# Optimization experiments

Measured on AMD Instinct MI355X. Metric: run time of the kernel, lower is better.

## Reference

```python
import jax, jax.numpy as jnp
import numpy as np

TEMP = 0.07
BASE_TEMP = 0.07
LOSS_WEIGHT = 0.5
BN_EPS = 1e-5


def _embed(x, w1, b1, gamma, beta, w2, b2):
    # 1x1 conv C->C  (x: [N,C,H,W], w1: [C_out,C_in])
    h = jnp.einsum('nchw,oc->nohw', x, w1) + b1[None, :, None, None]
    # BatchNorm2d in training mode: batch stats over (N,H,W), biased variance
    mean = h.mean(axis=(0, 2, 3), keepdims=True)
    var = h.var(axis=(0, 2, 3), keepdims=True)
    h = (h - mean) * jax.lax.rsqrt(var + BN_EPS)
    h = h * gamma[None, :, None, None] + beta[None, :, None, None]
    h = jax.nn.relu(h)
    h = jnp.einsum('nchw,oc->nohw', h, w2) + b2[None, :, None, None]
    # F.normalize(p=2, dim=1) with eps=1e-12
    nrm = jnp.sqrt(jnp.sum(h * h, axis=1, keepdims=True))
    return h / jnp.maximum(nrm, 1e-12)


def _contrastive(feats_, labels_):
    # feats_: [T, n_view, C]; labels_: [T]
    T, n_view, C = feats_.shape
    mask_small = (labels_[:, None] == labels_[None, :]).astype(feats_.dtype)  # [T,T]
    # torch.cat(torch.unbind(feats_, dim=1), dim=0): view-major ordering
    cf = feats_.transpose(1, 0, 2).reshape(T * n_view, C)
    logits = (cf @ cf.T) / TEMP                                   # [M,M], M=T*n_view
    logits = logits - jax.lax.stop_gradient(jnp.max(logits, axis=1, keepdims=True))
    mask = jnp.tile(mask_small, (n_view, n_view))                  # repeat(anchor_count, contrast_count)
    neg_mask = 1.0 - mask                                          # computed BEFORE diagonal removal
    M = T * n_view
    logits_mask = 1.0 - jnp.eye(M, dtype=feats_.dtype)
    mask = mask * logits_mask
    exp_logits = jnp.exp(logits)
    neg_logits = jnp.sum(exp_logits * neg_mask, axis=1, keepdims=True)
    log_prob = logits - jnp.log(exp_logits + neg_logits)
    mean_log_prob_pos = jnp.sum(mask * log_prob, axis=1) / (jnp.sum(mask, axis=1) + 1e-6)
    loss = -(TEMP / BASE_TEMP) * mean_log_prob_pos
    return jnp.mean(loss)


def setup_inputs() -> dict:
    N, C_in, H, W = 8, 512, 128, 128
    feat_dim, num_classes = 256, 19
    max_views, max_samples, ignore_label = 100, 1024, -1
    rng = np.random.RandomState(0)

    preds_S = rng.randn(N, C_in, H, W).astype(np.float32)
    # gt label map already at (H,W) => nearest interpolation is identity
    gt = rng.randint(0, num_classes, (N, H * W))
    logits_S = rng.randn(N, num_classes, H * W).astype(np.float32)
    predict = logits_S.argmax(axis=1)  # [N, H*W]

    # ---- replicate _hard_anchor_sampling on host (fixed seed) ----
    classes, total = [], 0
    for i in range(N):
        cl = [int(c) for c in np.unique(gt[i])
              if c != ignore_label and (gt[i] == c).sum() > max_views]
        classes.append(cl)
        total += len(cl)
    n_view = min(max_samples // total, max_views)

    b_idx, p_idx, y_cls = [], [], []
    for i in range(N):
        for c in classes[i]:
            hard = np.where((predict[i] == c) & (gt[i] != c))[0]
            easy = np.where((predict[i] == c) & (gt[i] == c))[0]
            nh, ne = len(hard), len(easy)
            if nh >= n_view / 2 and ne >= n_view / 2:
                kh = n_view // 2; ke = n_view - kh
            elif nh >= n_view / 2:
                ke = ne; kh = n_view - ke
            else:
                kh = nh; ke = n_view - kh
            hs = hard[rng.permutation(nh)[:kh]]
            es = easy[rng.permutation(ne)[:ke]]
            b_idx.append(i)
            p_idx.append(np.concatenate([hs, es]))
            y_cls.append(c)

    batch_idx = jnp.asarray(np.array(b_idx), dtype=jnp.int32)          # [T]
    pix_idx = jnp.asarray(np.stack(p_idx), dtype=jnp.int32)            # [T, n_view]
    y_cls = jnp.asarray(np.array(y_cls), dtype=jnp.int32)              # [T]

    def p(shape, scale, k):
        r = np.random.RandomState(k)
        return jnp.asarray((r.randn(*shape) * scale).astype(np.float32))

    return {
        'preds_S': jnp.asarray(preds_S),
        'w1': p((C_in, C_in), 0.02, 1),
        'b1': jnp.zeros((C_in,), jnp.float32),
        'gamma': jnp.ones((C_in,), jnp.float32),
        'beta': jnp.zeros((C_in,), jnp.float32),
        'w2': p((feat_dim, C_in), 0.02, 2),
        'b2': jnp.zeros((feat_dim,), jnp.float32),
        'batch_idx': batch_idx,
        'pix_idx': pix_idx,
        'y_cls': y_cls,
    }


def reference(preds_S, w1, b1, gamma, beta, w2, b2, batch_idx, pix_idx, y_cls):
    f = _embed(preds_S, w1, b1, gamma, beta, w2, b2)        # [N, C, H, W]
    N, C, H, W = f.shape
    feats = f.transpose(0, 2, 3, 1).reshape(N, H * W, C)     # [N, HW, C]
    X_ = feats[batch_idx[:, None], pix_idx]                   # [T, n_view, C]
    labels_ = y_cls.astype(f.dtype)
    return LOSS_WEIGHT * _contrastive(X_, labels_)
```

## Files before the change

kernel.cpp:

```cpp
#include <hip/hip_runtime.h>
#include <hip/hip_bf16.h>

#define C_IN   512
#define C_OUT  256
#define HW     16384
#define NIMG   8
#define PTOT   (NIMG * HW)
#define MP     1024
#define TEMP_INV (1.0f / 0.07f)
#define BN_EPS   1e-5f
#define SPB    4
#define OGRP   8
#define IGRP   4

typedef float  f32x4  __attribute__((ext_vector_type(4)));
typedef short  short8 __attribute__((ext_vector_type(8)));
typedef short  short4v __attribute__((ext_vector_type(4)));

#define WS_S1   0
#define WS_G    (WS_S1 + C_IN)
#define WS_W1P  (WS_G + C_IN * C_IN)
#define WS_B1P  (WS_W1P + C_IN * C_IN)
#define WS_CF   (WS_B1P + C_IN)
#define WS_XB_F (WS_CF + MP * C_OUT)
#define WS_NEED_FAST ((size_t)WS_XB_F * 4 + (size_t)PTOT * C_IN * 2)

__global__ __launch_bounds__(256)
void kprep(const float* __restrict__ x, __hip_bfloat16* __restrict__ xb,
           float* __restrict__ s1) {
    int plane = blockIdx.x;
    int c = plane & (C_IN - 1);
    const float4* p = (const float4*)(x + (size_t)plane * HW);
    short4v* q = (short4v*)(xb + (size_t)plane * HW);
    float acc = 0.f;
    for (int i = threadIdx.x; i < HW / 4; i += 256) {
        float4 v = p[i];
        acc += v.x + v.y + v.z + v.w;
        union { short4v s; __hip_bfloat162 h[2]; } u;
        u.h[0] = __float22bfloat162_rn(make_float2(v.x, v.y));
        u.h[1] = __float22bfloat162_rn(make_float2(v.z, v.w));
        q[i] = u.s;
    }
    for (int off = 32; off; off >>= 1) acc += __shfl_down(acc, off, 64);
    __shared__ float red[4];
    int lane = threadIdx.x & 63, wv = threadIdx.x >> 6;
    if (lane == 0) red[wv] = acc;
    __syncthreads();
    if (threadIdx.x == 0)
        atomicAdd(&s1[c], red[0] + red[1] + red[2] + red[3]);
}

__global__ __launch_bounds__(256)
void ksum(const float* __restrict__ x, float* __restrict__ s1) {
    int plane = blockIdx.x;
    int c = plane & (C_IN - 1);
    const float4* p = (const float4*)(x + (size_t)plane * HW);
    float acc = 0.f;
    for (int i = threadIdx.x; i < HW / 4; i += 256) {
        float4 v = p[i];
        acc += v.x + v.y + v.z + v.w;
    }
    for (int off = 32; off; off >>= 1) acc += __shfl_down(acc, off, 64);
    __shared__ float red[4];
    int lane = threadIdx.x & 63, wv = threadIdx.x >> 6;
    if (lane == 0) red[wv] = acc;
    __syncthreads();
    if (threadIdx.x == 0)
        atomicAdd(&s1[c], red[0] + red[1] + red[2] + red[3]);
}

__device__ const int TILE_I[10] = {0,0,0,0,1,1,1,2,2,3};
__device__ const int TILE_J[10] = {0,1,2,3,1,2,3,2,3,3};

__global__ __launch_bounds__(256, 2)
void kgram_bf16(const __hip_bfloat16* __restrict__ xb, float* __restrict__ G) {
    int tile  = blockIdx.x;
    int chunk = blockIdx.y;
    int n   = chunk >> 4;
    int hw0 = (chunk & 15) * 1024;
    int wave = threadIdx.x >> 6;
    int lane = threadIdx.x & 63;
    int wi = wave >> 1, wj = wave & 1;
    int I0 = TILE_I[tile] * 128 + wi * 64;
    int J0 = TILE_J[tile] * 128 + wj * 64;
    int m    = lane & 15;
    int koff = (lane >> 4) * 8;

    const __hip_bfloat16* rowA[4];
    const __hip_bfloat16* rowB[4];
#pragma unroll
    for (int t = 0; t < 4; ++t) {
        rowA[t] = xb + ((size_t)n * C_IN + (I0 + t * 16 + m)) * HW + hw0 + koff;
        rowB[t] = xb + ((size_t)n * C_IN + (J0 + t * 16 + m)) * HW + hw0 + koff;
    }

    f32x4 acc[4][4];
#pragma unroll
    for (int i = 0; i < 4; ++i)
#pragma unroll
        for (int j = 0; j < 4; ++j) acc[i][j] = {0.f, 0.f, 0.f, 0.f};

    short8 A0[4][2], B0[4][2], A1[4][2], B1[4][2];

#define LOADSTAGE(Ab, Bb, kk)                                              \
    {                                                                      \
        _Pragma("unroll")                                                  \
        for (int t = 0; t < 4; ++t) {                                      \
            Ab[t][0] = *(const short8*)(rowA[t] + (kk));                   \
            Ab[t][1] = *(const short8*)(rowA[t] + (kk) + 32);              \
            Bb[t][0] = *(const short8*)(rowB[t] + (kk));                   \
            Bb[t][1] = *(const short8*)(rowB[t] + (kk) + 32);              \
        }                                                                  \
    }
#define MFMASTAGE(Ab, Bb)                                                  \
    {                                                                      \
        _Pragma("unroll")                                                  \
        for (int u = 0; u < 2; ++u)                                        \
            _Pragma("unroll")                                              \
            for (int i = 0; i < 4; ++i)                                    \
                _Pragma("unroll")                                          \
                for (int j = 0; j < 4; ++j)                                \
                    acc[i][j] = __builtin_amdgcn_mfma_f32_16x16x32_bf16(   \
                        Ab[i][u], Bb[j][u], acc[i][j], 0, 0, 0);           \
    }

    LOADSTAGE(A0, B0, 0)
    int kk = 0;
#pragma unroll 1
    for (int s = 0; s < 7; ++s) {
        LOADSTAGE(A1, B1, kk + 64)
        MFMASTAGE(A0, B0)
        LOADSTAGE(A0, B0, kk + 128)
        MFMASTAGE(A1, B1)
        kk += 128;
    }
    LOADSTAGE(A1, B1, kk + 64)
    MFMASTAGE(A0, B0)
    MFMASTAGE(A1, B1)
#undef LOADSTAGE
#undef MFMASTAGE

    int r0 = (lane >> 4) * 4;
    int cc = lane & 15;
#pragma unroll
    for (int i = 0; i < 4; ++i)
#pragma unroll
        for (int j = 0; j < 4; ++j)
#pragma unroll
            for (int r = 0; r < 4; ++r)
                atomicAdd(&G[(size_t)(I0 + i * 16 + r0 + r) * C_IN + (J0 + j * 16 + cc)],
                          acc[i][j][r]);
}

__global__ __launch_bounds__(256)
void kmirror(float* __restrict__ G) {
    int i = blockIdx.x;
    for (int j = threadIdx.x; j < C_IN; j += 256) {
        if ((i >> 7) > (j >> 7))
            G[(size_t)i * C_IN + j] = G[(size_t)j * C_IN + i];
    }
}

__device__ inline short8 load_frag_f32(const float* p) {
    float4 a = *(const float4*)p;
    float4 b = *(const float4*)(p + 4);
    union { short8 s; __hip_bfloat162 h[4]; } u;
    u.h[0] = __float22bfloat162_rn(make_float2(a.x, a.y));
    u.h[1] = __float22bfloat162_rn(make_float2(a.z, a.w));
    u.h[2] = __float22bfloat162_rn(make_float2(b.x, b.y));
    u.h[3] = __float22bfloat162_rn(make_float2(b.z, b.w));
    return u.s;
}

__global__ __launch_bounds__(256)
void kgram_f32(const float* __restrict__ x, float* __restrict__ G) {
    int bz  = blockIdx.z;
    int n   = bz >> 2;
    int hw0 = (bz & 3) * 4096;
    int wave = threadIdx.x >> 6;
    int lane = threadIdx.x & 63;
    int wi = wave >> 1, wj = wave & 1;
    int I0 = blockIdx.x * 128 + wi * 64;
    int J0 = blockIdx.y * 128 + wj * 64;
    int m    = lane & 15;
    int koff = (lane >> 4) * 8;

    const float* baseA[4];
    const float* baseB[4];
#pragma unroll
    for (int t = 0; t < 4; ++t) {
        baseA[t] = x + ((size_t)n * C_IN + (I0 + t * 16 + m)) * HW + hw0 + koff;
        baseB[t] = x + ((size_t)n * C_IN + (J0 + t * 16 + m)) * HW + hw0 + koff;
    }

    f32x4 acc[4][4];
#pragma unroll
    for (int i = 0; i < 4; ++i)
#pragma unroll
        for (int j = 0; j < 4; ++j) acc[i][j] = {0.f, 0.f, 0.f, 0.f};

    for (int kk = 0; kk < 4096; kk += 32) {
        short8 afr[4], bfr[4];
#pragma unroll
        for (int t = 0; t < 4; ++t) {
            afr[t] = load_frag_f32(baseA[t] + kk);
            bfr[t] = load_frag_f32(baseB[t] + kk);
        }
#pragma unroll
        for (int i = 0; i < 4; ++i)
#pragma unroll
            for (int j = 0; j < 4; ++j)
                acc[i][j] = __builtin_amdgcn_mfma_f32_16x16x32_bf16(
                    afr[i], bfr[j], acc[i][j], 0, 0, 0);
    }

    int r0 = (lane >> 4) * 4;
    int cc = lane & 15;
#pragma unroll
    for (int i = 0; i < 4; ++i)
#pragma unroll
        for (int j = 0; j < 4; ++j)
#pragma unroll
            for (int r = 0; r < 4; ++r)
                atomicAdd(&G[(size_t)(I0 + i * 16 + r0 + r) * C_IN + (J0 + j * 16 + cc)],
                          acc[i][j][r]);
}

__global__ __launch_bounds__(256)
void kstats(const float* __restrict__ w1, const float* __restrict__ b1,
            const float* __restrict__ gamma, const float* __restrict__ beta,
            const float* __restrict__ s1, const float* __restrict__ G,
            float* __restrict__ w1p, float* __restrict__ b1p) {
    int o0 = blockIdx.x * OGRP;
    int tid = threadIdx.x;
    __shared__ float wr[OGRP][C_IN];
    __shared__ float redd[4][OGRP];
    __shared__ float redq[4][OGRP];
    __shared__ float alpha_s[OGRP];

    for (int idx = tid; idx < OGRP * C_IN; idx += 256) {
        int og = idx >> 9, c = idx & (C_IN - 1);
        wr[og][c] = w1[(size_t)(o0 + og) * C_IN + c];
    }
    __syncthreads();

    float dot1[OGRP], quad[OGRP];
#pragma unroll
    for (int og = 0; og < OGRP; ++og) { dot1[og] = 0.f; quad[og] = 0.f; }

    for (int c = tid; c < C_IN; c += 256) {
        const float* gr = G + (size_t)c * C_IN;
        float s1c = s1[c];
        float inner[OGRP];
#pragma unroll
        for (int og = 0; og < OGRP; ++og) inner[og] = 0.f;
        for (int d = 0; d < C_IN; d += 4) {
            float4 gv = *(const float4*)(gr + d);
#pragma unroll
            for (int og = 0; og < OGRP; ++og) {
                float4 wv = *(const float4*)(&wr[og][d]);
                inner[og] += gv.x * wv.x + gv.y * wv.y + gv.z * wv.z + gv.w * wv.w;
            }
        }
#pragma unroll
        for (int og = 0; og < OGRP; ++og) {
            float wc = wr[og][c];
            quad[og] += inner[og] * wc;
            dot1[og] += s1c * wc;
        }
    }
#pragma unroll
    for (int og = 0; og < OGRP; ++og) {
        for (int off = 32; off; off >>= 1) {
            dot1[og] += __shfl_down(dot1[og], off, 64);
            quad[og] += __shfl_down(quad[og], off, 64);
        }
    }
    int lane = tid & 63, wv = tid >> 6;
    if (lane == 0) {
#pragma unroll
        for (int og = 0; og < OGRP; ++og) { redd[wv][og] = dot1[og]; redq[wv][og] = quad[og]; }
    }
    __syncthreads();
    if (tid < OGRP) {
        int og = tid;
        float d1 = redd[0][og] + redd[1][og] + redd[2][og] + redd[3][og];
        float q  = redq[0][og] + redq[1][og] + redq[2][og] + redq[3][og];
        float b  = b1[o0 + og];
        float mean = d1 / (float)PTOT + b;
        float eh2  = (q + 2.f * b * d1) / (float)PTOT + b * b;
        float var  = eh2 - mean * mean;
        float al   = gamma[o0 + og] * rsqrtf(var + BN_EPS);
        alpha_s[og] = al;
        b1p[o0 + og] = beta[o0 + og] + al * (b - mean);
    }
    __syncthreads();
    for (int idx = tid; idx < OGRP * C_IN; idx += 256) {
        int og = idx >> 9, c = idx & (C_IN - 1);
        w1p[(size_t)(o0 + og) * C_IN + c] = alpha_s[og] * wr[og][c];
    }
}

__global__ __launch_bounds__(256)
void kfeat(const float* __restrict__ x, const float* __restrict__ w1p,
           const float* __restrict__ b1p, const float* __restrict__ w2,
           const float* __restrict__ b2, const int* __restrict__ batch_idx,
           const int* __restrict__ pix_idx, float* __restrict__ cf,
           int M, int T, int n_view) {
    __shared__ float xcol[SPB][C_IN];
    __shared__ float h1[SPB][C_IN];
    __shared__ float fl[SPB][C_OUT];
    int tid = threadIdx.x;
    int m0 = blockIdx.x * SPB;

    for (int idx = tid; idx < SPB * C_IN; idx += 256) {
        int s = idx >> 9, c = idx & (C_IN - 1);
        int mm = m0 + s;
        float v = 0.f;
        if (mm < M) {
            int t = mm % T, vv = mm / T;
            int n = batch_idx[t];
            int pix = pix_idx[t * n_view + vv];
            v = x[((size_t)n * C_IN + c) * HW + pix];
        }
        xcol[s][c] = v;
    }
    __syncthreads();

    for (int o = tid; o < C_IN; o += 256) {
        float acc[SPB];
        float bb = b1p[o];
#pragma unroll
        for (int s = 0; s < SPB; ++s) acc[s] = bb;
        const float* wrp = w1p + (size_t)o * C_IN;
        for (int c = 0; c < C_IN; ++c) {
            float w = wrp[c];
#pragma unroll
            for (int s = 0; s < SPB; ++s) acc[s] += w * xcol[s][c];
        }
#pragma unroll
        for (int s = 0; s < SPB; ++s) h1[s][o] = fmaxf(acc[s], 0.f);
    }
    __syncthreads();

    {
        int j = tid;
        float acc[SPB];
        float bb = b2[j];
#pragma unroll
        for (int s = 0; s < SPB; ++s) acc[s] = bb;
        const float* wrp = w2 + (size_t)j * C_IN;
        for (int o = 0; o < C_IN; ++o) {
            float w = wrp[o];
#pragma unroll
            for (int s = 0; s < SPB; ++s) acc[s] += w * h1[s][o];
        }
#pragma unroll
        for (int s = 0; s < SPB; ++s) fl[s][j] = acc[s];
    }
    __syncthreads();

    int wv = tid >> 6, lane = tid & 63;
    {
        float sq = 0.f;
#pragma unroll
        for (int k = 0; k < 4; ++k) { float v = fl[wv][lane + 64 * k]; sq += v * v; }
        for (int off = 32; off; off >>= 1) sq += __shfl_down(sq, off, 64);
        float nrm = __shfl(sq, 0, 64);
        float rinv = 1.f / fmaxf(sqrtf(nrm), 1e-12f);
        int mm = m0 + wv;
        if (mm < M) {
#pragma unroll
            for (int k = 0; k < 4; ++k)
                cf[(size_t)mm * C_OUT + lane + 64 * k] = fl[wv][lane + 64 * k] * rinv;
        }
    }
}

__global__ __launch_bounds__(256)
void kloss(const float* __restrict__ cf, const int* __restrict__ y_cls,
           float* __restrict__ out, int M, int T) {
    int i0 = blockIdx.x * IGRP;
    int tid = threadIdx.x;
    __shared__ float ci[IGRP][C_OUT];
    __shared__ float row[IGRP][MP];
    __shared__ int   lbl[MP];
    __shared__ float redl[IGRP];
    int lane = tid & 63, wv = tid >> 6;

    for (int idx = tid; idx < IGRP * C_OUT; idx += 256) {
        int g = idx >> 8, c = idx & (C_OUT - 1);
        int ii = i0 + g;
        ci[g][c] = (ii < M) ? cf[(size_t)ii * C_OUT + c] : 0.f;
    }
    for (int j = tid; j < M; j += 256) lbl[j] = y_cls[j % T];
    __syncthreads();

    for (int j = tid; j < M; j += 256) {
        const float* cj = cf + (size_t)j * C_OUT;
        float acc[IGRP];
#pragma unroll
        for (int g = 0; g < IGRP; ++g) acc[g] = 0.f;
        for (int c = 0; c < C_OUT; c += 4) {
            float4 v = *(const float4*)(cj + c);
#pragma unroll
            for (int g = 0; g < IGRP; ++g) {
                float4 cv = *(const float4*)(&ci[g][c]);
                acc[g] += cv.x * v.x + cv.y * v.y + cv.z * v.z + cv.w * v.w;
            }
        }
#pragma unroll
        for (int g = 0; g < IGRP; ++g) row[g][j] = acc[g] * TEMP_INV;
    }
    __syncthreads();

    int i = i0 + wv;
    if (i < M) {
        int lbl_i = lbl[i];
        const float* r = row[wv];

        float mx = -1e30f;
        for (int j = lane; j < M; j += 64) mx = fmaxf(mx, r[j]);
        for (int off = 32; off; off >>= 1) mx = fmaxf(mx, __shfl_down(mx, off, 64));
        mx = __shfl(mx, 0, 64);

        float neg = 0.f;
        for (int j = lane; j < M; j += 64)
            if (lbl[j] != lbl_i) neg += expf(r[j] - mx);
        for (int off = 32; off; off >>= 1) neg += __shfl_down(neg, off, 64);
        neg = __shfl(neg, 0, 64);

        float pos = 0.f; int cnt = 0;
        for (int j = lane; j < M; j += 64) {
            if (lbl[j] == lbl_i && j != i) {
                float l = r[j] - mx;
                pos += l - logf(expf(l) + neg);
                cnt++;
            }
        }
        for (int off = 32; off; off >>= 1) {
            pos += __shfl_down(pos, off, 64);
            cnt += __shfl_down(cnt, off, 64);
        }
        if (lane == 0) redl[wv] = -pos / ((float)cnt + 1e-6f);
    } else if (lane == 0) redl[wv] = 0.f;
    __syncthreads();
    if (tid == 0) {
        float s = redl[0] + redl[1] + redl[2] + redl[3];
        atomicAdd(out, s * (0.5f / (float)M));
    }
}

extern "C" void kernel_launch(void* const* d_in, const int* in_sizes, int n_in,
                              void* d_out, int out_size, void* d_ws, size_t ws_size,
                              hipStream_t stream) {
    const float* x     = (const float*)d_in[0];
    const float* w1    = (const float*)d_in[1];
    const float* b1    = (const float*)d_in[2];
    const float* gamma = (const float*)d_in[3];
    const float* beta  = (const float*)d_in[4];
    const float* w2    = (const float*)d_in[5];
    const float* b2    = (const float*)d_in[6];
    const int* batch_idx = (const int*)d_in[7];
    const int* pix_idx   = (const int*)d_in[8];
    const int* y_cls     = (const int*)d_in[9];

    int T = in_sizes[7];
    int M = in_sizes[8];
    int n_view = M / T;

    float* ws  = (float*)d_ws;
    float* s1  = ws + WS_S1;
    float* G   = ws + WS_G;
    float* w1p = ws + WS_W1P;
    float* b1p = ws + WS_B1P;
    float* cf  = ws + WS_CF;
    __hip_bfloat16* xb = (__hip_bfloat16*)(ws + WS_XB_F);

    hipMemsetAsync(s1, 0, (size_t)(C_IN + C_IN * C_IN) * sizeof(float), stream);
    hipMemsetAsync(d_out, 0, sizeof(float), stream);

    if (ws_size >= WS_NEED_FAST) {
        kprep<<<NIMG * C_IN, 256, 0, stream>>>(x, xb, s1);
        kgram_bf16<<<dim3(10, 128), 256, 0, stream>>>(xb, G);
        kmirror<<<C_IN, 256, 0, stream>>>(G);
    } else {
        ksum<<<NIMG * C_IN, 256, 0, stream>>>(x, s1);
        kgram_f32<<<dim3(4, 4, 32), 256, 0, stream>>>(x, G);
    }
    kstats<<<C_IN / OGRP, 256, 0, stream>>>(w1, b1, gamma, beta, s1, G, w1p, b1p);
    kfeat<<<(M + SPB - 1) / SPB, 256, 0, stream>>>(x, w1p, b1p, w2, b2,
                                                   batch_idx, pix_idx, cf, M, T, n_view);
    kloss<<<(M + IGRP - 1) / IGRP, 256, 0, stream>>>(cf, y_cls, (float*)d_out, M, T);
}
```

Baseline: 769.9 us.

## Stage Gram tiles through swizzled LDS via direct global-to-LDS loads

The bf16 Gram kernel used to load MFMA fragments straight from global memory into registers, so each wave re-read rows that other waves in the block also needed. It now copies each 128-row A/B tile into double-buffered, XOR-swizzled shared memory with global_load_lds, and the waves read their fragments from LDS. This cuts redundant global traffic but adds a barrier per K step and 64KB of LDS, which may limit occupancy. Separately, the contrastive-loss kernel now handles 8 anchor rows per block instead of 4.

```diff
diff --git a/kernel.cpp b/kernel.cpp
--- a/kernel.cpp
+++ b/kernel.cpp
@@ -11,7 +11,8 @@
 #define BN_EPS   1e-5f
 #define SPB    4
 #define OGRP   8
-#define IGRP   4
+#define IGRP   8
+#define BK     64
 
 typedef float  f32x4  __attribute__((ext_vector_type(4)));
 typedef short  short8 __attribute__((ext_vector_type(8)));
@@ -74,6 +75,8 @@
 
 __global__ __launch_bounds__(256, 2)
 void kgram_bf16(const __hip_bfloat16* __restrict__ xb, float* __restrict__ G) {
+    __shared__ __hip_bfloat16 Abuf[2][128 * BK];
+    __shared__ __hip_bfloat16 Bbuf[2][128 * BK];
     int tile  = blockIdx.x;
     int chunk = blockIdx.y;
     int n   = chunk >> 4;
@@ -81,18 +84,14 @@
     int wave = threadIdx.x >> 6;
     int lane = threadIdx.x & 63;
     int wi = wave >> 1, wj = wave & 1;
-    int I0 = TILE_I[tile] * 128 + wi * 64;
-    int J0 = TILE_J[tile] * 128 + wj * 64;
-    int m    = lane & 15;
-    int koff = (lane >> 4) * 8;
-
-    const __hip_bfloat16* rowA[4];
-    const __hip_bfloat16* rowB[4];
-#pragma unroll
-    for (int t = 0; t < 4; ++t) {
-        rowA[t] = xb + ((size_t)n * C_IN + (I0 + t * 16 + m)) * HW + hw0 + koff;
-        rowB[t] = xb + ((size_t)n * C_IN + (J0 + t * 16 + m)) * HW + hw0 + koff;
-    }
+    int IT = TILE_I[tile] * 128;
+    int JT = TILE_J[tile] * 128;
+
+    const __hip_bfloat16* gA = xb + ((size_t)n * C_IN + IT) * HW + hw0;
+    const __hip_bfloat16* gB = xb + ((size_t)n * C_IN + JT) * HW + hw0;
+
+    int rrel = lane >> 3;
+    int slot = lane & 7;
 
     f32x4 acc[4][4];
 #pragma unroll
@@ -100,45 +99,66 @@
 #pragma unroll
         for (int j = 0; j < 4; ++j) acc[i][j] = {0.f, 0.f, 0.f, 0.f};
 
-    short8 A0[4][2], B0[4][2], A1[4][2], B1[4][2];
-
-#define LOADSTAGE(Ab, Bb, kk)                                              \
-    {                                                                      \
-        _Pragma("unroll")                                                  \
-        for (int t = 0; t < 4; ++t) {                                      \
-            Ab[t][0] = *(const short8*)(rowA[t] + (kk));                   \
-            Ab[t][1] = *(const short8*)(rowA[t] + (kk) + 32);              \
-            Bb[t][0] = *(const short8*)(rowB[t] + (kk));                   \
-            Bb[t][1] = *(const short8*)(rowB[t] + (kk) + 32);              \
-        }                                                                  \
-    }
-#define MFMASTAGE(Ab, Bb)                                                  \
-    {                                                                      \
-        _Pragma("unroll")                                                  \
-        for (int u = 0; u < 2; ++u)                                        \
-            _Pragma("unroll")                                              \
-            for (int i = 0; i < 4; ++i)                                    \
-                _Pragma("unroll")                                          \
-                for (int j = 0; j < 4; ++j)                                \
-                    acc[i][j] = __builtin_amdgcn_mfma_f32_16x16x32_bf16(   \
-                        Ab[i][u], Bb[j][u], acc[i][j], 0, 0, 0);           \
-    }
-
-    LOADSTAGE(A0, B0, 0)
-    int kk = 0;
+    int m  = lane & 15;
+    int kq = lane >> 4;
+
+#define STAGE(s, pb)                                                          \
+    {                                                                         \
+        int kk_ = (s) * BK;                                                   \
+        _Pragma("unroll")                                                     \
+        for (int i_ = 0; i_ < 4; ++i_) {                                      \
+            int row_ = wave * 32 + i_ * 8 + rrel;                             \
+            int g_   = slot ^ (row_ & 7);                                     \
+            __builtin_amdgcn_global_load_lds(                                 \
+                (const __attribute__((address_space(1))) void*)               \
+                    (gA + (size_t)row_ * HW + kk_ + g_ * 8),                  \
+                (__attribute__((address_space(3))) void*)                     \
+                    (&Abuf[pb][(wave * 32 + i_ * 8) * BK]),                   \
+                16, 0, 0);                                                    \
+            __builtin_amdgcn_global_load_lds(                                 \
+                (const __attribute__((address_space(1))) void*)               \
+                    (gB + (size_t)row_ * HW + kk_ + g_ * 8),                  \
+                (__attribute__((address_space(3))) void*)                     \
+                    (&Bbuf[pb][(wave * 32 + i_ * 8) * BK]),                   \
+                16, 0, 0);                                                    \
+        }                                                                     \
+    }
+
+#define COMPUTE(pb)                                                           \
+    {                                                                         \
+        _Pragma("unroll")                                                     \
+        for (int h_ = 0; h_ < 2; ++h_) {                                      \
+            short8 af_[4], bf_[4];                                            \
+            _Pragma("unroll")                                                 \
+            for (int t_ = 0; t_ < 4; ++t_) {                                  \
+                int ra_ = wi * 64 + t_ * 16 + m;                              \
+                int qa_ = (h_ * 4 + kq) ^ (ra_ & 7);                          \
+                af_[t_] = *(const short8*)&Abuf[pb][ra_ * BK + qa_ * 8];      \
+                int rb_ = wj * 64 + t_ * 16 + m;                              \
+                int qb_ = (h_ * 4 + kq) ^ (rb_ & 7);                          \
+                bf_[t_] = *(const short8*)&Bbuf[pb][rb_ * BK + qb_ * 8];      \
+            }                                                                 \
+            _Pragma("unroll")                                                 \
+            for (int i_ = 0; i_ < 4; ++i_)                                    \
+                _Pragma("unroll")                                             \
+                for (int j_ = 0; j_ < 4; ++j_)                                \
+                    acc[i_][j_] = __builtin_amdgcn_mfma_f32_16x16x32_bf16(    \
+                        af_[i_], bf_[j_], acc[i_][j_], 0, 0, 0);              \
+        }                                                                     \
+    }
+
+    STAGE(0, 0)
+    __syncthreads();
+    int pb = 0;
 #pragma unroll 1
-    for (int s = 0; s < 7; ++s) {
-        LOADSTAGE(A1, B1, kk + 64)
-        MFMASTAGE(A0, B0)
-        LOADSTAGE(A0, B0, kk + 128)
-        MFMASTAGE(A1, B1)
-        kk += 128;
-    }
-    LOADSTAGE(A1, B1, kk + 64)
-    MFMASTAGE(A0, B0)
-    MFMASTAGE(A1, B1)
-#undef LOADSTAGE
-#undef MFMASTAGE
+    for (int s = 0; s < 16; ++s) {
+        if (s < 15) STAGE(s + 1, pb ^ 1)
+        COMPUTE(pb)
+        __syncthreads();
+        pb ^= 1;
+    }
+#undef STAGE
+#undef COMPUTE
 
     int r0 = (lane >> 4) * 4;
     int cc = lane & 15;
@@ -148,7 +168,8 @@
         for (int j = 0; j < 4; ++j)
 #pragma unroll
             for (int r = 0; r < 4; ++r)
-                atomicAdd(&G[(size_t)(I0 + i * 16 + r0 + r) * C_IN + (J0 + j * 16 + cc)],
+                atomicAdd(&G[(size_t)(IT + wi * 64 + i * 16 + r0 + r) * C_IN
+                             + (JT + wj * 64 + j * 16 + cc)],
                           acc[i][j][r]);
 }
 
@@ -414,39 +435,42 @@
     }
     __syncthreads();
 
-    int i = i0 + wv;
-    if (i < M) {
-        int lbl_i = lbl[i];
-        const float* r = row[wv];
-
-        float mx = -1e30f;
-        for (int j = lane; j < M; j += 64) mx = fmaxf(mx, r[j]);
-        for (int off = 32; off; off >>= 1) mx = fmaxf(mx, __shfl_down(mx, off, 64));
-        mx = __shfl(mx, 0, 64);
-
-        float neg = 0.f;
-        for (int j = lane; j < M; j += 64)
-            if (lbl[j] != lbl_i) neg += expf(r[j] - mx);
-        for (int off = 32; off; off >>= 1) neg += __shfl_down(neg, off, 64);
-        neg = __shfl(neg, 0, 64);
-
-        float pos = 0.f; int cnt = 0;
-        for (int j = lane; j < M; j += 64) {
-            if (lbl[j] == lbl_i && j != i) {
-                float l = r[j] - mx;
-                pos += l - logf(expf(l) + neg);
-                cnt++;
+    for (int g = wv; g < IGRP; g += 4) {
+        int i = i0 + g;
+        if (i < M) {
+            int lbl_i = lbl[i];
+            const float* r = row[g];
+
+            float mx = -1e30f;
+            for (int j = lane; j < M; j += 64) mx = fmaxf(mx, r[j]);
+            for (int off = 32; off; off >>= 1) mx = fmaxf(mx, __shfl_down(mx, off, 64));
+            mx = __shfl(mx, 0, 64);
+
+            float neg = 0.f;
+            for (int j = lane; j < M; j += 64)
+                if (lbl[j] != lbl_i) neg += expf(r[j] - mx);
+            for (int off = 32; off; off >>= 1) neg += __shfl_down(neg, off, 64);
+            neg = __shfl(neg, 0, 64);
+
+            float pos = 0.f; int cnt = 0;
+            for (int j = lane; j < M; j += 64) {
+                if (lbl[j] == lbl_i && j != i) {
+                    float l = r[j] - mx;
+                    pos += l - logf(expf(l) + neg);
+                    cnt++;
+                }
             }
-        }
-        for (int off = 32; off; off >>= 1) {
-            pos += __shfl_down(pos, off, 64);
-            cnt += __shfl_down(cnt, off, 64);
-        }
-        if (lane == 0) redl[wv] = -pos / ((float)cnt + 1e-6f);
-    } else if (lane == 0) redl[wv] = 0.f;
+            for (int off = 32; off; off >>= 1) {
+                pos += __shfl_down(pos, off, 64);
+                cnt += __shfl_down(cnt, off, 64);
+            }
+            if (lane == 0) redl[g] = -pos / ((float)cnt + 1e-6f);
+        } else if (lane == 0) redl[g] = 0.f;
+    }
     __syncthreads();
     if (tid == 0) {
-        float s = redl[0] + redl[1] + redl[2] + redl[3];
+        float s = 0.f;
+        for (int g = 0; g < IGRP; ++g) s += redl[g];
         atomicAdd(out, s * (0.5f / (float)M));
     }
 }
```

Result: faster. 706.2 us (-8.3%).
